# Kernel tuning notes

Hardware: AMD Instinct MI355X
Metric: run time of the kernel (lower is better)

Reference implementation:

```python
import jax, jax.numpy as jnp
import numpy as np

EMBED_DIM = 192
KERNEL_MUL = 2.0
KERNEL_NUM = 5


def setup_inputs() -> dict:
    key = jax.random.key(0)
    k1, k2, k3 = jax.random.split(key, 3)
    x = jax.random.normal(k1, (8192, EMBED_DIM), dtype=jnp.float32)
    label = jax.random.randint(k2, (8192,), 0, 1000, dtype=jnp.int32)
    genre_label = jax.random.randint(k3, (8192,), 0, 8, dtype=jnp.int32)
    return {"x": x, "label": label, "genre_label": genre_label}


def reference(x, label, genre_label):
    # even rows -> source, odd rows -> target (label/genre_label unused by the loss)
    source = x[::2].reshape(-1, EMBED_DIM)
    target = x[1::2].reshape(-1, EMBED_DIM)
    total = jnp.concatenate([source, target], axis=0)  # [N, D]
    n = total.shape[0]
    n_samples = n  # source rows + target rows

    # pairwise squared L2 via ||a||^2 + ||b||^2 - 2 a.b (avoids N x N x D buffer)
    sq = jnp.sum(total * total, axis=1)  # [N]
    L2 = sq[:, None] + sq[None, :] - 2.0 * (total @ total.T)  # [N, N]
    L2 = jnp.maximum(L2, 0.0)

    # bandwidth from detached distances (matches torch .data)
    bandwidth = jax.lax.stop_gradient(jnp.sum(L2)) / (n_samples ** 2 - n_samples)
    bandwidth = bandwidth / (KERNEL_MUL ** (KERNEL_NUM // 2))

    # multi-bandwidth RBF kernel sum
    kernels = jnp.zeros_like(L2)
    for i in range(KERNEL_NUM):
        kernels = kernels + jnp.exp(-L2 / (bandwidth * (KERNEL_MUL ** i)))

    x_n = source.shape[0]
    y_n = target.shape[0]
    xx = kernels[:x_n, :x_n]
    yy = kernels[y_n:, y_n:]
    xy = kernels[:x_n, y_n:]
    yx = kernels[y_n:, :x_n]
    loss = jnp.mean(xx + yy - xy - yx)
    return loss
```

## Files before the change

### kernel.cpp

```cpp
#include <hip/hip_runtime.h>
#include <math.h>

#define N_TOTAL 8192
#define HALF    4096
#define EMBED   192
#define BT      128
#define NT      (N_TOTAL / BT)
#define NBLK    (NT * (NT + 1) / 2)

typedef short bf16x8 __attribute__((ext_vector_type(8)));
typedef float f32x4  __attribute__((ext_vector_type(4)));


__device__ __forceinline__ unsigned pack2_bf16(float a, float b) {
    unsigned ua = __float_as_uint(a), ub = __float_as_uint(b);
    unsigned ha = (ua + 0x7FFFu + ((ua >> 16) & 1u)) >> 16;
    unsigned hb = (ub + 0x7FFFu + ((ub >> 16) & 1u)) >> 16;
    return ha | (hb << 16);
}

__global__ __launch_bounds__(256) void prep(
    const float* __restrict__ x, unsigned short* __restrict__ xb,
    float* __restrict__ sq, float* __restrict__ colsum,
    double* __restrict__ sumsq_all) {
    __shared__ float  ls_col[EMBED];
    __shared__ double ls_sq[4];
    int t = threadIdx.x;
    if (t < EMBED) ls_col[t] = 0.f;
    __syncthreads();

    int r   = blockIdx.x * 32 + (t >> 3);
    int sub = t & 7;
    int g   = (r & 1) ? (HALF + (r >> 1)) : (r >> 1);
    const float*    src = x  + (size_t)r * EMBED;
    unsigned short* dst = xb + (size_t)g * EMBED;

    float  s = 0.f;
    float4 v[6];
#pragma unroll
    for (int m = 0; m < 6; ++m) {
        v[m] = *(const float4*)(src + (sub + 8 * m) * 4);
        s += v[m].x * v[m].x + v[m].y * v[m].y + v[m].z * v[m].z + v[m].w * v[m].w;
    }
#pragma unroll
    for (int m = 0; m < 6; ++m) {
        uint2 o;
        o.x = pack2_bf16(v[m].x, v[m].y);
        o.y = pack2_bf16(v[m].z, v[m].w);
        *(uint2*)(dst + (sub + 8 * m) * 4) = o;
    }
    s += __shfl_xor(s, 1, 64);
    s += __shfl_xor(s, 2, 64);
    s += __shfl_xor(s, 4, 64);
    if (sub == 0) sq[g] = s;
#pragma unroll
    for (int m = 0; m < 6; ++m) {
        int c = (sub + 8 * m) * 4;
        atomicAdd(&ls_col[c + 0], v[m].x);
        atomicAdd(&ls_col[c + 1], v[m].y);
        atomicAdd(&ls_col[c + 2], v[m].z);
        atomicAdd(&ls_col[c + 3], v[m].w);
    }
    float bs = (sub == 0) ? s : 0.f;
    bs += __shfl_xor(bs, 8, 64);
    bs += __shfl_xor(bs, 16, 64);
    bs += __shfl_xor(bs, 32, 64);
    if ((t & 63) == 0) ls_sq[t >> 6] = (double)bs;
    __syncthreads();
    if (t < EMBED) atomicAdd(&colsum[t], ls_col[t]);
    if (t == 0) atomicAdd(sumsq_all, ls_sq[0] + ls_sq[1] + ls_sq[2] + ls_sq[3]);
}

__global__ __launch_bounds__(256) void finalize_bw(
    const float* __restrict__ colsum, const double* __restrict__ sumsq_all,
    float* __restrict__ inv_c) {
    __shared__ double ws[4];
    int t = threadIdx.x;
    double c = (t < EMBED) ? (double)colsum[t] : 0.0;
    double p = c * c;
#pragma unroll
    for (int off = 32; off; off >>= 1) p += __shfl_down(p, off, 64);
    if ((t & 63) == 0) ws[t >> 6] = p;
    __syncthreads();
    if (t == 0) {
        double s2 = ws[0] + ws[1] + ws[2] + ws[3];
        double n  = (double)N_TOTAL;
        double sumL2 = 2.0 * n * (*sumsq_all) - 2.0 * s2;
        double bw = sumL2 / (n * n - n) / 4.0;
        *inv_c = (float)(1.0 / (16.0 * bw));
    }
}

__global__ __launch_bounds__(256, 3) void mmd_mfma(
    const unsigned short* __restrict__ xb, const float* __restrict__ sq,
    const float* __restrict__ inv_c, double* __restrict__ acc_out) {
    int id = blockIdx.x, bi = 0;
    while (id >= NT - bi) { id -= NT - bi; ++bi; }
    int bj = bi + id;
    int I0 = bi * BT, J0 = bj * BT;

    __shared__ double wred[4];

    int t = threadIdx.x, lane = t & 63, wid = t >> 6;
    int wy = (wid >> 1) * 64, wx = (wid & 1) * 64;
    int lo = lane & 15, kg = lane >> 4;

    const unsigned short* pA = xb + (size_t)(I0 + wy + lo) * EMBED + kg * 8;
    const unsigned short* pB = xb + (size_t)(J0 + wx + lo) * EMBED + kg * 8;

    f32x4 acc[4][4];
#pragma unroll
    for (int i = 0; i < 4; ++i)
#pragma unroll
        for (int j = 0; j < 4; ++j) acc[i][j] = (f32x4)(0.f);

#pragma unroll
    for (int kk = 0; kk < EMBED; kk += 32) {
        bf16x8 a[4], b[4];
#pragma unroll
        for (int i = 0; i < 4; ++i) a[i] = *(const bf16x8*)(pA + i * 16 * EMBED + kk);
#pragma unroll
        for (int j = 0; j < 4; ++j) b[j] = *(const bf16x8*)(pB + j * 16 * EMBED + kk);
#pragma unroll
        for (int i = 0; i < 4; ++i)
#pragma unroll
            for (int j = 0; j < 4; ++j)
                acc[i][j] = __builtin_amdgcn_mfma_f32_16x16x32_bf16(a[i], b[j], acc[i][j], 0, 0, 0);
    }

    const float cc = *inv_c;
    int gi0 = I0 + wy + kg * 4;
    int gj0 = J0 + wx + lo;
    float sqi[4][4], sqj[4];
#pragma unroll
    for (int i = 0; i < 4; ++i)
#pragma unroll
        for (int r = 0; r < 4; ++r) sqi[i][r] = sq[gi0 + i * 16 + r];
#pragma unroll
    for (int j = 0; j < 4; ++j) sqj[j] = sq[gj0 + j * 16];

    float sgn  = ((bi < NT / 2) == (bj < NT / 2)) ? 1.f : -1.f;
    float tsum = 0.f;
    if (bi != bj) {
#pragma unroll
        for (int i = 0; i < 4; ++i)
#pragma unroll
            for (int j = 0; j < 4; ++j)
#pragma unroll
                for (int r = 0; r < 4; ++r) {
                    float L2 = sqi[i][r] + sqj[j] - 2.f * acc[i][j][r];
                    L2 = fmaxf(L2, 0.f);
                    float u   = __expf(-L2 * cc);
                    float u2  = u * u;
                    float u4  = u2 * u2;
                    float u8  = u4 * u4;
                    float u16 = u8 * u8;
                    tsum += (u + u2 + u4 + u8 + u16);
                }
        tsum *= 2.f;
    } else {
#pragma unroll
        for (int i = 0; i < 4; ++i)
#pragma unroll
            for (int j = 0; j < 4; ++j)
#pragma unroll
                for (int r = 0; r < 4; ++r) {
                    int gi = gi0 + i * 16 + r, gj = gj0 + j * 16;
                    float w = (gi < gj) ? 2.f : ((gi == gj) ? 1.f : 0.f);
                    float L2 = sqi[i][r] + sqj[j] - 2.f * acc[i][j][r];
                    L2 = fmaxf(L2, 0.f);
                    float u   = __expf(-L2 * cc);
                    float u2  = u * u;
                    float u4  = u2 * u2;
                    float u8  = u4 * u4;
                    float u16 = u8 * u8;
                    tsum += w * (u + u2 + u4 + u8 + u16);
                }
    }
    tsum *= sgn;

#pragma unroll
    for (int off = 32; off; off >>= 1) tsum += __shfl_down(tsum, off, 64);
    if (lane == 0) wred[wid] = (double)tsum;
    __syncthreads();
    if (t == 0) atomicAdd(acc_out, wred[0] + wred[1] + wred[2] + wred[3]);
}

__global__ void finalize_loss(const double* __restrict__ acc, float* __restrict__ out) {
    if (threadIdx.x == 0 && blockIdx.x == 0)
        out[0] = (float)(*acc / ((double)HALF * (double)HALF));
}

extern "C" void kernel_launch(void* const* d_in, const int* in_sizes, int n_in,
                              void* d_out, int out_size, void* d_ws, size_t ws_size,
                              hipStream_t stream) {
    const float* x = (const float*)d_in[0];

    double*         d_sumsq  = (double*)d_ws;
    double*         d_acc    = (double*)d_ws + 1;
    float*          d_colsum = (float*)((char*)d_ws + 16);
    float*          d_invc   = (float*)((char*)d_ws + 784);
    float*          d_sq     = (float*)((char*)d_ws + 800);
    unsigned short* d_xb     = (unsigned short*)((char*)d_ws + 33568);

    hipMemsetAsync(d_ws, 0, 800, stream);

    prep<<<N_TOTAL / 32, 256, 0, stream>>>(x, d_xb, d_sq, d_colsum, d_sumsq);
    finalize_bw<<<1, 256, 0, stream>>>(d_colsum, d_sumsq, d_invc);
    mmd_mfma<<<NBLK, 256, 0, stream>>>(d_xb, d_sq, d_invc, d_acc);
    finalize_loss<<<1, 1, 0, stream>>>(d_acc, (float*)d_out);
}
```

Before: 135.9 us.

## Stage MFMA tiles via LDS, fuse bandwidth into prep, exp2 epilogue, per-block partials

```diff
diff --git a/kernel.cpp b/kernel.cpp
--- a/kernel.cpp
+++ b/kernel.cpp
@@ -7,9 +7,13 @@
 #define BT      128
 #define NT      (N_TOTAL / BT)
 #define NBLK    (NT * (NT + 1) / 2)
-
-typedef short bf16x8 __attribute__((ext_vector_type(8)));
-typedef float f32x4  __attribute__((ext_vector_type(4)));
+#define KC      64
+#define NPREP   256
+#define LOG2E   1.4426950408889634f
+
+typedef short          bf16x8 __attribute__((ext_vector_type(8)));
+typedef float          f32x4  __attribute__((ext_vector_type(4)));
+typedef unsigned short ushort_t;
 
 
 __device__ __forceinline__ unsigned pack2_bf16(float a, float b) {
@@ -20,20 +24,21 @@
 }
 
 __global__ __launch_bounds__(256) void prep(
-    const float* __restrict__ x, unsigned short* __restrict__ xb,
-    float* __restrict__ sq, float* __restrict__ colsum,
-    double* __restrict__ sumsq_all) {
-    __shared__ float  ls_col[EMBED];
-    __shared__ double ls_sq[4];
-    int t = threadIdx.x;
-    if (t < EMBED) ls_col[t] = 0.f;
-    __syncthreads();
-
-    int r   = blockIdx.x * 32 + (t >> 3);
-    int sub = t & 7;
-    int g   = (r & 1) ? (HALF + (r >> 1)) : (r >> 1);
-    const float*    src = x  + (size_t)r * EMBED;
-    unsigned short* dst = xb + (size_t)g * EMBED;
+    const float* __restrict__ x, ushort_t* __restrict__ xb,
+    float* __restrict__ sq, float* __restrict__ colpart,
+    double* __restrict__ sqpart, int* __restrict__ counter,
+    float* __restrict__ ccl_out) {
+    __shared__ float4 lscol[4][48];
+    __shared__ double lssq[4];
+    __shared__ int    lastflag;
+    __shared__ double red[4][2];
+
+    int t = threadIdx.x, b = blockIdx.x;
+    int lane = t & 63, w = t >> 6;
+    int r = b * 32 + (t >> 3), sub = t & 7;
+    int g = (r & 1) ? (HALF + (r >> 1)) : (r >> 1);
+    const float* src = x  + (size_t)r * EMBED;
+    ushort_t*    dst = xb + (size_t)g * EMBED;
 
     float  s = 0.f;
     float4 v[6];
@@ -55,58 +60,87 @@
     if (sub == 0) sq[g] = s;
 #pragma unroll
     for (int m = 0; m < 6; ++m) {
-        int c = (sub + 8 * m) * 4;
-        atomicAdd(&ls_col[c + 0], v[m].x);
-        atomicAdd(&ls_col[c + 1], v[m].y);
-        atomicAdd(&ls_col[c + 2], v[m].z);
-        atomicAdd(&ls_col[c + 3], v[m].w);
+#pragma unroll
+        for (int off = 8; off <= 32; off <<= 1) {
+            v[m].x += __shfl_xor(v[m].x, off, 64);
+            v[m].y += __shfl_xor(v[m].y, off, 64);
+            v[m].z += __shfl_xor(v[m].z, off, 64);
+            v[m].w += __shfl_xor(v[m].w, off, 64);
+        }
+    }
+    if (lane < 8) {
+#pragma unroll
+        for (int m = 0; m < 6; ++m) lscol[w][lane + 8 * m] = v[m];
     }
     float bs = (sub == 0) ? s : 0.f;
     bs += __shfl_xor(bs, 8, 64);
     bs += __shfl_xor(bs, 16, 64);
     bs += __shfl_xor(bs, 32, 64);
-    if ((t & 63) == 0) ls_sq[t >> 6] = (double)bs;
-    __syncthreads();
-    if (t < EMBED) atomicAdd(&colsum[t], ls_col[t]);
-    if (t == 0) atomicAdd(sumsq_all, ls_sq[0] + ls_sq[1] + ls_sq[2] + ls_sq[3]);
-}
-
-__global__ __launch_bounds__(256) void finalize_bw(
-    const float* __restrict__ colsum, const double* __restrict__ sumsq_all,
-    float* __restrict__ inv_c) {
-    __shared__ double ws[4];
-    int t = threadIdx.x;
-    double c = (t < EMBED) ? (double)colsum[t] : 0.0;
-    double p = c * c;
-#pragma unroll
-    for (int off = 32; off; off >>= 1) p += __shfl_down(p, off, 64);
-    if ((t & 63) == 0) ws[t >> 6] = p;
+    if (lane == 0) lssq[w] = (double)bs;
+    __syncthreads();
+    if (t < 48) {
+        float4 a = lscol[0][t], b4 = lscol[1][t], c4 = lscol[2][t], d4 = lscol[3][t];
+        float4 o;
+        o.x = a.x + b4.x + c4.x + d4.x;
+        o.y = a.y + b4.y + c4.y + d4.y;
+        o.z = a.z + b4.z + c4.z + d4.z;
+        o.w = a.w + b4.w + c4.w + d4.w;
+        ((float4*)colpart)[b * 48 + t] = o;
+    }
+    if (t == 0) sqpart[b] = lssq[0] + lssq[1] + lssq[2] + lssq[3];
+
+    __threadfence();
     __syncthreads();
     if (t == 0) {
-        double s2 = ws[0] + ws[1] + ws[2] + ws[3];
-        double n  = (double)N_TOTAL;
-        double sumL2 = 2.0 * n * (*sumsq_all) - 2.0 * s2;
+        int old = atomicAdd(counter, 1);
+        lastflag = (old == NPREP - 1);
+    }
+    __syncthreads();
+    if (!lastflag) return;
+    __threadfence();
+
+    double p = 0.0;
+    if (t < EMBED) {
+        float cs = 0.f;
+        for (int bb = 0; bb < NPREP; ++bb) cs += colpart[bb * EMBED + t];
+        p = (double)cs * (double)cs;
+    }
+    double z = sqpart[t];
+#pragma unroll
+    for (int off = 32; off; off >>= 1) {
+        p += __shfl_down(p, off, 64);
+        z += __shfl_down(z, off, 64);
+    }
+    if (lane == 0) { red[w][0] = p; red[w][1] = z; }
+    __syncthreads();
+    if (t == 0) {
+        double P = red[0][0] + red[1][0] + red[2][0] + red[3][0];
+        double S = red[0][1] + red[1][1] + red[2][1] + red[3][1];
+        double n = (double)N_TOTAL;
+        double sumL2 = 2.0 * n * S - 2.0 * P;
         double bw = sumL2 / (n * n - n) / 4.0;
-        *inv_c = (float)(1.0 / (16.0 * bw));
-    }
-}
-
-__global__ __launch_bounds__(256, 3) void mmd_mfma(
-    const unsigned short* __restrict__ xb, const float* __restrict__ sq,
-    const float* __restrict__ inv_c, double* __restrict__ acc_out) {
+        *ccl_out = (float)((double)LOG2E / (16.0 * bw));
+    }
+}
+
+__global__ __launch_bounds__(256, 4) void mmd_mfma(
+    const ushort_t* __restrict__ xb, const float* __restrict__ sq,
+    const float* __restrict__ ccl_p, double* __restrict__ accpart) {
     int id = blockIdx.x, bi = 0;
     while (id >= NT - bi) { id -= NT - bi; ++bi; }
     int bj = bi + id;
     int I0 = bi * BT, J0 = bj * BT;
 
-    __shared__ double wred[4];
+    __shared__ ushort_t As[BT][KC];
+    __shared__ ushort_t Bs[BT][KC];
+    __shared__ double   wred[4];
 
     int t = threadIdx.x, lane = t & 63, wid = t >> 6;
     int wy = (wid >> 1) * 64, wx = (wid & 1) * 64;
     int lo = lane & 15, kg = lane >> 4;
 
-    const unsigned short* pA = xb + (size_t)(I0 + wy + lo) * EMBED + kg * 8;
-    const unsigned short* pB = xb + (size_t)(J0 + wx + lo) * EMBED + kg * 8;
+    int srow = lane >> 3;
+    int sch  = (lane & 7) ^ srow;
 
     f32x4 acc[4][4];
 #pragma unroll
@@ -114,30 +148,49 @@
 #pragma unroll
         for (int j = 0; j < 4; ++j) acc[i][j] = (f32x4)(0.f);
 
-#pragma unroll
-    for (int kk = 0; kk < EMBED; kk += 32) {
-        bf16x8 a[4], b[4];
-#pragma unroll
-        for (int i = 0; i < 4; ++i) a[i] = *(const bf16x8*)(pA + i * 16 * EMBED + kk);
-#pragma unroll
-        for (int j = 0; j < 4; ++j) b[j] = *(const bf16x8*)(pB + j * 16 * EMBED + kk);
-#pragma unroll
-        for (int i = 0; i < 4; ++i)
-#pragma unroll
-            for (int j = 0; j < 4; ++j)
-                acc[i][j] = __builtin_amdgcn_mfma_f32_16x16x32_bf16(a[i], b[j], acc[i][j], 0, 0, 0);
-    }
-
-    const float cc = *inv_c;
+    const float ccl = *ccl_p;
+
+    for (int c = 0; c < 3; ++c) {
+        int kc0 = c * KC;
+#pragma unroll
+        for (int qi = 0; qi < 8; ++qi) {
+            int q    = wid * 8 + qi;
+            int row0 = (q & 15) * 8;
+            int grow = ((q >> 4) ? J0 : I0) + row0 + srow;
+            const ushort_t* gp = xb + (size_t)grow * EMBED + kc0 + sch * 8;
+            ushort_t* lp = ((q >> 4) ? &Bs[0][0] : &As[0][0]) + row0 * KC;
+            __builtin_amdgcn_global_load_lds(
+                (const __attribute__((address_space(1))) void*)gp,
+                (__attribute__((address_space(3))) void*)lp, 16, 0, 0);
+        }
+        __syncthreads();
+#pragma unroll
+        for (int kh = 0; kh < 2; ++kh) {
+            int ch = ((kh << 2) + kg) ^ (lo & 7);
+            bf16x8 a[4], b[4];
+#pragma unroll
+            for (int i = 0; i < 4; ++i) a[i] = *(const bf16x8*)&As[wy + i * 16 + lo][ch * 8];
+#pragma unroll
+            for (int j = 0; j < 4; ++j) b[j] = *(const bf16x8*)&Bs[wx + j * 16 + lo][ch * 8];
+#pragma unroll
+            for (int i = 0; i < 4; ++i)
+#pragma unroll
+                for (int j = 0; j < 4; ++j)
+                    acc[i][j] = __builtin_amdgcn_mfma_f32_16x16x32_bf16(a[i], b[j], acc[i][j], 0, 0, 0);
+        }
+        __syncthreads();
+    }
+
     int gi0 = I0 + wy + kg * 4;
     int gj0 = J0 + wx + lo;
-    float sqi[4][4], sqj[4];
+    float nsic[4][4], nsjc[4];
 #pragma unroll
     for (int i = 0; i < 4; ++i)
 #pragma unroll
-        for (int r = 0; r < 4; ++r) sqi[i][r] = sq[gi0 + i * 16 + r];
-#pragma unroll
-    for (int j = 0; j < 4; ++j) sqj[j] = sq[gj0 + j * 16];
+        for (int r = 0; r < 4; ++r) nsic[i][r] = -ccl * sq[gi0 + i * 16 + r];
+#pragma unroll
+    for (int j = 0; j < 4; ++j) nsjc[j] = -ccl * sq[gj0 + j * 16];
+    const float cc2 = 2.f * ccl;
 
     float sgn  = ((bi < NT / 2) == (bj < NT / 2)) ? 1.f : -1.f;
     float tsum = 0.f;
@@ -148,14 +201,10 @@
             for (int j = 0; j < 4; ++j)
 #pragma unroll
                 for (int r = 0; r < 4; ++r) {
-                    float L2 = sqi[i][r] + sqj[j] - 2.f * acc[i][j][r];
-                    L2 = fmaxf(L2, 0.f);
-                    float u   = __expf(-L2 * cc);
-                    float u2  = u * u;
-                    float u4  = u2 * u2;
-                    float u8  = u4 * u4;
-                    float u16 = u8 * u8;
-                    tsum += (u + u2 + u4 + u8 + u16);
+                    float arg = fminf(fmaf(cc2, acc[i][j][r], nsic[i][r]) + nsjc[j], 0.f);
+                    float u   = exp2f(arg);
+                    float u2 = u * u, u4 = u2 * u2, u8 = u4 * u4, u16 = u8 * u8;
+                    tsum += ((u + u2) + (u4 + u8)) + u16;
                 }
         tsum *= 2.f;
     } else {
@@ -167,14 +216,10 @@
                 for (int r = 0; r < 4; ++r) {
                     int gi = gi0 + i * 16 + r, gj = gj0 + j * 16;
                     float w = (gi < gj) ? 2.f : ((gi == gj) ? 1.f : 0.f);
-                    float L2 = sqi[i][r] + sqj[j] - 2.f * acc[i][j][r];
-                    L2 = fmaxf(L2, 0.f);
-                    float u   = __expf(-L2 * cc);
-                    float u2  = u * u;
-                    float u4  = u2 * u2;
-                    float u8  = u4 * u4;
-                    float u16 = u8 * u8;
-                    tsum += w * (u + u2 + u4 + u8 + u16);
+                    float arg = fminf(fmaf(cc2, acc[i][j][r], nsic[i][r]) + nsjc[j], 0.f);
+                    float u   = exp2f(arg);
+                    float u2 = u * u, u4 = u2 * u2, u8 = u4 * u4, u16 = u8 * u8;
+                    tsum += w * (((u + u2) + (u4 + u8)) + u16);
                 }
     }
     tsum *= sgn;
@@ -183,12 +228,23 @@
     for (int off = 32; off; off >>= 1) tsum += __shfl_down(tsum, off, 64);
     if (lane == 0) wred[wid] = (double)tsum;
     __syncthreads();
-    if (t == 0) atomicAdd(acc_out, wred[0] + wred[1] + wred[2] + wred[3]);
-}
-
-__global__ void finalize_loss(const double* __restrict__ acc, float* __restrict__ out) {
-    if (threadIdx.x == 0 && blockIdx.x == 0)
-        out[0] = (float)(*acc / ((double)HALF * (double)HALF));
+    if (t == 0) accpart[blockIdx.x] = wred[0] + wred[1] + wred[2] + wred[3];
+}
+
+__global__ __launch_bounds__(256) void finalize_loss(
+    const double* __restrict__ accpart, float* __restrict__ out) {
+    __shared__ double red[4];
+    int t = threadIdx.x, lane = t & 63, w = t >> 6;
+    double s = 0.0;
+    for (int i = t; i < NBLK; i += 256) s += accpart[i];
+#pragma unroll
+    for (int off = 32; off; off >>= 1) s += __shfl_down(s, off, 64);
+    if (lane == 0) red[w] = s;
+    __syncthreads();
+    if (t == 0) {
+        double tot = red[0] + red[1] + red[2] + red[3];
+        out[0] = (float)(tot / ((double)HALF * (double)HALF));
+    }
 }
 
 extern "C" void kernel_launch(void* const* d_in, const int* in_sizes, int n_in,
@@ -196,17 +252,18 @@
                               hipStream_t stream) {
     const float* x = (const float*)d_in[0];
 
-    double*         d_sumsq  = (double*)d_ws;
-    double*         d_acc    = (double*)d_ws + 1;
-    float*          d_colsum = (float*)((char*)d_ws + 16);
-    float*          d_invc   = (float*)((char*)d_ws + 784);
-    float*          d_sq     = (float*)((char*)d_ws + 800);
-    unsigned short* d_xb     = (unsigned short*)((char*)d_ws + 33568);
-
-    hipMemsetAsync(d_ws, 0, 800, stream);
-
-    prep<<<N_TOTAL / 32, 256, 0, stream>>>(x, d_xb, d_sq, d_colsum, d_sumsq);
-    finalize_bw<<<1, 256, 0, stream>>>(d_colsum, d_sumsq, d_invc);
-    mmd_mfma<<<NBLK, 256, 0, stream>>>(d_xb, d_sq, d_invc, d_acc);
-    finalize_loss<<<1, 1, 0, stream>>>(d_acc, (float*)d_out);
-}
+    int*      d_counter = (int*)d_ws;
+    float*    d_ccl     = (float*)((char*)d_ws + 8);
+    float*    d_sq      = (float*)((char*)d_ws + 1024);
+    ushort_t* d_xb      = (ushort_t*)((char*)d_ws + 33792);
+    float*    d_colpart = (float*)((char*)d_ws + 3179520);
+    double*   d_sqpart  = (double*)((char*)d_ws + 3376128);
+    double*   d_accpart = (double*)((char*)d_ws + 3378176);
+
+    hipMemsetAsync(d_ws, 0, 1024, stream);
+
+    prep<<<NPREP, 256, 0, stream>>>(x, d_xb, d_sq, d_colpart, d_sqpart,
+                                    d_counter, d_ccl);
+    mmd_mfma<<<NBLK, 256, 0, stream>>>(d_xb, d_sq, d_ccl, d_accpart);
+    finalize_loss<<<1, 256, 0, stream>>>(d_accpart, (float*)d_out);
+}
```

Result: faster. 121.9 us (-10.3%).
